# Optimization experiments

Hardware: AMD Instinct MI355X
Metric: run time of the kernel (lower is better)

Reference implementation:

```python
import jax, jax.numpy as jnp
import numpy as np

E, H, PV, RD, NS, SP, T = 4, 64, 300, 64, 8, 6, 2
N = 5000
IN_GRU = 2 * E * H  # 512


def layer_norm(x, g, b, eps=1e-5):
    m = jnp.mean(x, axis=-1, keepdims=True)
    v = jnp.var(x, axis=-1, keepdims=True)
    return (x - m) * jax.lax.rsqrt(v + eps) * g + b


def setup_inputs() -> dict:
    key = jax.random.key(0)
    ks = jax.random.split(key, 32)
    s = 0.05
    inp = {
        'adjacency_matrix': (jax.random.uniform(ks[0], (E, N, N), jnp.float32) < 0.01).astype(jnp.float32),
        'node_states': jax.random.normal(ks[1], (N, NS), jnp.float32),
        'node_ids': jnp.arange(N, dtype=jnp.int32),
        'node_vectors': jax.random.normal(ks[2], (N, PV), jnp.float32),
        'node_size_and_pos': jax.random.normal(ks[3], (N, SP), jnp.float32),
        # reduce_dimentionality: Linear(300,64)+Tanh
        'W_red': jax.random.normal(ks[4], (PV, RD), jnp.float32) * s,
        'b_red': jnp.zeros((RD,), jnp.float32),
        # node_init2hidden: Linear(64+8+6,64)+Tanh
        'W_init': jax.random.normal(ks[5], (RD + NS + SP, H), jnp.float32) * s,
        'b_init': jnp.zeros((H,), jnp.float32),
        # per-edge-type message FCs (stacked over edge types)
        'W_out': jax.random.normal(ks[6], (E, H, H), jnp.float32) * s,
        'b_out': jnp.zeros((E, H), jnp.float32),
        'W_in_e': jax.random.normal(ks[7], (E, H, H), jnp.float32) * s,
        'b_in_e': jnp.zeros((E, H), jnp.float32),
        # LayerNormGRUCell(2*E*H, H)
        'W_ih_rz': jax.random.normal(ks[8], (IN_GRU, 2 * H), jnp.float32) * s,
        'b_ih_rz': jnp.zeros((2 * H,), jnp.float32),
        'W_hh_rz': jax.random.normal(ks[9], (H, 2 * H), jnp.float32) * s,
        'b_hh_rz': jnp.zeros((2 * H,), jnp.float32),
        'W_ih_c': jax.random.normal(ks[10], (IN_GRU, H), jnp.float32) * s,
        'b_ih_c': jnp.zeros((H,), jnp.float32),
        'W_hh_c': jax.random.normal(ks[11], (H, H), jnp.float32) * s,
        'b_hh_c': jnp.zeros((H,), jnp.float32),
        'g_i2h': jnp.ones((2 * H,), jnp.float32), 'be_i2h': jnp.zeros((2 * H,), jnp.float32),
        'g_h2h': jnp.ones((2 * H,), jnp.float32), 'be_h2h': jnp.zeros((2 * H,), jnp.float32),
        'g_ci': jnp.ones((H,), jnp.float32), 'be_ci': jnp.zeros((H,), jnp.float32),
        'g_ch': jnp.ones((H,), jnp.float32), 'be_ch': jnp.zeros((H,), jnp.float32),
    }
    return inp


def _messages(A, h, W, b):
    # per-edge-type FC + tanh: [E,N,H]
    hs = jnp.tanh(jnp.einsum('nh,ehk->enk', h, W) + b[:, None, :])
    # adjacency matmul per edge type: [E,N,N] @ [E,N,H] -> [E,N,H]
    m = jnp.einsum('enm,emh->enh', A, hs)
    # torch.stack(list,1).view(N,-1) == [N, E*H]
    return jnp.transpose(m, (1, 0, 2)).reshape(h.shape[0], E * H)


def reference(adjacency_matrix, node_states, node_ids, node_vectors, node_size_and_pos,
              W_red, b_red, W_init, b_init, W_out, b_out, W_in_e, b_in_e,
              W_ih_rz, b_ih_rz, W_hh_rz, b_hh_rz, W_ih_c, b_ih_c, W_hh_c, b_hh_c,
              g_i2h, be_i2h, g_h2h, be_h2h, g_ci, be_ci, g_ch, be_ch):
    emb = jnp.tanh(node_vectors @ W_red + b_red)                      # [N,RD]
    node_init = jnp.concatenate([emb, node_states, node_size_and_pos], axis=1)
    h = jnp.tanh(node_init @ W_init + b_init)                          # [N,H]
    A_out = adjacency_matrix
    A_in = jnp.transpose(adjacency_matrix, (0, 2, 1))
    for _ in range(T):
        m_out = _messages(A_out, h, W_out, b_out)                      # [N,E*H]
        m_in = _messages(A_in, h, W_in_e, b_in_e)                      # [N,E*H]
        msg = jnp.concatenate([m_out, m_in], axis=1)                   # [N,2EH]
        # LayerNormGRUCell
        rz = jax.nn.sigmoid(layer_norm(msg @ W_ih_rz + b_ih_rz, g_i2h, be_i2h)
                            + layer_norm(h @ W_hh_rz + b_hh_rz, g_h2h, be_h2h))
        r, z = rz[:, :H], rz[:, H:]
        c = jnp.tanh(layer_norm(msg @ W_ih_c + b_ih_c, g_ci, be_ci)
                     + r * layer_norm(h @ W_hh_c + b_hh_c, g_ch, be_ch))
        h = z * h + (1.0 - z) * c
    return h
```

## Files before the change

kernel.cpp:

```cpp
#include <hip/hip_runtime.h>
#include <math.h>

#define N    5000
#define E    4
#define H    64
#define PV   300
#define RD   64
#define NS_  8
#define SP_  6
#define NI   (RD + NS_ + SP_)
#define GH   (2 * H)
#define MSGW (2 * E * H)
#define CAP  128
#define NPB  8
#define MSG_BPS 256

#define PK_S0 ((MSGW / 4) * GH)
#define PK_S1 ((MSGW / 4) * H)
#define PK_S2 ((H / 4) * GH)
#define PK_S3 ((H / 4) * H)
#define PK_TOT (PK_S0 + PK_S1 + PK_S2 + PK_S3)

#define PRE_PACK_B 108
#define PRE_ZERO_B 40
#define PRE_INIT_B 313
#define PRE_GRID (PRE_PACK_B + PRE_ZERO_B + PRE_INIT_B)

__device__ __forceinline__ float wsum(float v) {
    v += __shfl_xor(v, 32, 64);
    v += __shfl_xor(v, 16, 64);
    v += __shfl_xor(v, 8, 64);
    v += __shfl_xor(v, 4, 64);
    v += __shfl_xor(v, 2, 64);
    v += __shfl_xor(v, 1, 64);
    return v;
}

__global__ __launch_bounds__(256) void k_pre(
    const float* __restrict__ Wih_rz, const float* __restrict__ Wih_c,
    const float* __restrict__ Whh_rz, const float* __restrict__ Whh_c,
    float4* __restrict__ Prz, float4* __restrict__ Pc,
    float4* __restrict__ Phrz, float4* __restrict__ Phc,
    int4* __restrict__ cnts,
    const float* __restrict__ NV, const float* __restrict__ NSt,
    const float* __restrict__ SPos, const float* __restrict__ Wred,
    const float* __restrict__ bred, const float* __restrict__ Winit,
    const float* __restrict__ binit, float* __restrict__ h)
{
    __shared__ float nv[16 * PV];
    __shared__ float ni[16 * NI];
    const int b = blockIdx.x;
    const int tid = threadIdx.x;

    if (b < PRE_PACK_B) {
        const int i = b * 256 + tid;
        if (i < PK_S0) {
            const int kq = i / GH, col = i - kq * GH;
            Prz[i] = make_float4(Wih_rz[(4 * kq + 0) * GH + col],
                                 Wih_rz[(4 * kq + 1) * GH + col],
                                 Wih_rz[(4 * kq + 2) * GH + col],
                                 Wih_rz[(4 * kq + 3) * GH + col]);
        } else if (i < PK_S0 + PK_S1) {
            const int t = i - PK_S0;
            const int kq = t / H, col = t - kq * H;
            Pc[t] = make_float4(Wih_c[(4 * kq + 0) * H + col],
                                Wih_c[(4 * kq + 1) * H + col],
                                Wih_c[(4 * kq + 2) * H + col],
                                Wih_c[(4 * kq + 3) * H + col]);
        } else if (i < PK_S0 + PK_S1 + PK_S2) {
            const int t = i - PK_S0 - PK_S1;
            const int kq = t / GH, col = t - kq * GH;
            Phrz[t] = make_float4(Whh_rz[(4 * kq + 0) * GH + col],
                                  Whh_rz[(4 * kq + 1) * GH + col],
                                  Whh_rz[(4 * kq + 2) * GH + col],
                                  Whh_rz[(4 * kq + 3) * GH + col]);
        } else {
            const int t = i - PK_S0 - PK_S1 - PK_S2;
            const int kq = t / H, col = t - kq * H;
            Phc[t] = make_float4(Whh_c[(4 * kq + 0) * H + col],
                                 Whh_c[(4 * kq + 1) * H + col],
                                 Whh_c[(4 * kq + 2) * H + col],
                                 Whh_c[(4 * kq + 3) * H + col]);
        }
    } else if (b < PRE_PACK_B + PRE_ZERO_B) {
        const int i = (b - PRE_PACK_B) * 256 + tid;
        if (i < (2 * E * N) / 4) cnts[i] = make_int4(0, 0, 0, 0);
    } else {
        const int n0 = (b - PRE_PACK_B - PRE_ZERO_B) * 16;
        const int j = tid & 63;
        const int w = tid >> 6;
        const int nb = w * 4;

        for (int idx = tid; idx < 16 * PV; idx += 256) {
            const int n = n0 + idx / PV;
            nv[idx] = (n < N) ? NV[(size_t)n0 * PV + idx] : 0.f;
        }
        __syncthreads();

        float acc[4];
        {
            const float br = bred[j];
            #pragma unroll
            for (int nn = 0; nn < 4; ++nn) acc[nn] = br;
        }
        for (int k = 0; k < PV; ++k) {
            const float wg = Wred[k * RD + j];
            #pragma unroll
            for (int nn = 0; nn < 4; ++nn) acc[nn] += nv[(nb + nn) * PV + k] * wg;
        }
        #pragma unroll
        for (int nn = 0; nn < 4; ++nn) ni[(nb + nn) * NI + j] = tanhf(acc[nn]);
        if (j < NS_) {
            #pragma unroll
            for (int nn = 0; nn < 4; ++nn) {
                const int n = n0 + nb + nn;
                ni[(nb + nn) * NI + RD + j] = (n < N) ? NSt[(size_t)n * NS_ + j] : 0.f;
            }
        }
        if (j < SP_) {
            #pragma unroll
            for (int nn = 0; nn < 4; ++nn) {
                const int n = n0 + nb + nn;
                ni[(nb + nn) * NI + RD + NS_ + j] = (n < N) ? SPos[(size_t)n * SP_ + j] : 0.f;
            }
        }
        __syncthreads();

        float a2[4];
        {
            const float bi = binit[j];
            #pragma unroll
            for (int nn = 0; nn < 4; ++nn) a2[nn] = bi;
        }
        for (int k = 0; k < NI; ++k) {
            const float wg = Winit[k * H + j];
            #pragma unroll
            for (int nn = 0; nn < 4; ++nn) a2[nn] += ni[(nb + nn) * NI + k] * wg;
        }
        #pragma unroll
        for (int nn = 0; nn < 4; ++nn) {
            const int n = n0 + nb + nn;
            if (n < N) h[(size_t)n * H + j] = tanhf(a2[nn]);
        }
    }
}

__global__ __launch_bounds__(256) void k_build(
    const float* __restrict__ A, int* __restrict__ cnt_out, int* __restrict__ cnt_in,
    unsigned short* __restrict__ idx_out, unsigned short* __restrict__ idx_in)
{
    const int r = blockIdx.x;
    const int e = r / N;
    const int n = r - e * N;
    __shared__ int s_cnt;
    __shared__ int s_cols[CAP];
    if (threadIdx.x == 0) s_cnt = 0;
    __syncthreads();

    const float4* row = (const float4*)(A + (size_t)r * N);
    const int lane = threadIdx.x & 63;
    #pragma unroll
    for (int it = 0; it < 3; ++it) {
        const int c0 = threadIdx.x + it * 512;
        const int c1 = c0 + 256;
        float4 v0 = make_float4(0.f, 0.f, 0.f, 0.f);
        float4 v1 = make_float4(0.f, 0.f, 0.f, 0.f);
        if (c0 < N / 4) v0 = row[c0];
        if (c1 < N / 4) v1 = row[c1];
        #pragma unroll
        for (int half = 0; half < 2; ++half) {
            const float4 v = half ? v1 : v0;
            const int c = half ? c1 : c0;
            #pragma unroll
            for (int comp = 0; comp < 4; ++comp) {
                const float val = (comp == 0) ? v.x : (comp == 1) ? v.y : (comp == 2) ? v.z : v.w;
                const bool p = (val != 0.f);
                const unsigned long long m = __ballot(p);
                if (m) {
                    int base = 0;
                    if (lane == 0) base = atomicAdd(&s_cnt, (int)__popcll(m));
                    base = __shfl(base, 0, 64);
                    if (p) {
                        const int pos = base + (int)__popcll(m & ((1ull << lane) - 1ull));
                        if (pos < CAP) s_cols[pos] = 4 * c + comp;
                    }
                }
            }
        }
    }
    __syncthreads();
    const int cnt = min(s_cnt, CAP);
    if (threadIdx.x == 0) cnt_out[r] = cnt;
    for (int i = threadIdx.x; i < cnt; i += 256)
        idx_out[(size_t)r * CAP + i] = (unsigned short)s_cols[i];
    for (int i = threadIdx.x; i < cnt; i += 256) {
        const int m = s_cols[i];
        const int p = atomicAdd(&cnt_in[e * N + m], 1);
        if (p < CAP) idx_in[(size_t)(e * N + m) * CAP + p] = (unsigned short)n;
    }
}

__global__ __launch_bounds__(256) void k_hs(
    const float* __restrict__ h, const float* __restrict__ Wout,
    const float* __restrict__ bout, const float* __restrict__ Win,
    const float* __restrict__ bin, float* __restrict__ hs_out,
    float* __restrict__ hs_in)
{
    __shared__ float hsd[8 * H];
    const int n0 = blockIdx.x * 8;
    const int tid = threadIdx.x;
    const int e = tid >> 6, j = tid & 63;

    for (int idx = tid; idx < 8 * H; idx += 256) hsd[idx] = h[(size_t)n0 * H + idx];
    __syncthreads();

    float aO[8], aI[8];
    {
        const float bO = bout[e * H + j], bI = bin[e * H + j];
        #pragma unroll
        for (int nn = 0; nn < 8; ++nn) { aO[nn] = bO; aI[nn] = bI; }
    }
    for (int k = 0; k < H; ++k) {
        const float wo = Wout[(e * H + k) * H + j];
        const float wi = Win[(e * H + k) * H + j];
        #pragma unroll
        for (int nn = 0; nn < 8; ++nn) {
            const float hv = hsd[nn * H + k];
            aO[nn] += hv * wo;
            aI[nn] += hv * wi;
        }
    }
    #pragma unroll
    for (int nn = 0; nn < 8; ++nn) {
        hs_out[((size_t)e * N + n0 + nn) * H + j] = tanhf(aO[nn]);
        hs_in[((size_t)e * N + n0 + nn) * H + j]  = tanhf(aI[nn]);
    }
}

__global__ __launch_bounds__(256) void k_msg(
    const float* __restrict__ hs_out, const float* __restrict__ hs_in,
    const int* __restrict__ cnt_out, const int* __restrict__ cnt_in,
    const unsigned short* __restrict__ idx_out, const unsigned short* __restrict__ idx_in,
    float* __restrict__ msg)
{
    const int slice = blockIdx.x & 7;
    const int sb = blockIdx.x >> 3;
    const int dir = slice >> 2;
    const int e = slice & 3;
    const int tid = threadIdx.x;
    const int wv = tid >> 6;
    const int lane = tid & 63;
    const int g = lane >> 4;
    const int l = lane & 15;

    const float4* hs4 = (const float4*)((dir ? hs_in : hs_out) + (size_t)e * N * H);
    const int* cnt = (dir ? cnt_in : cnt_out) + e * N;
    const unsigned short* idx = (dir ? idx_in : idx_out) + (size_t)e * N * CAP;
    float4* mdst = (float4*)msg;

    for (int n = sb * 4 + wv; n < N; n += MSG_BPS * 4) {
        const int c = min(cnt[n], CAP);
        const unsigned short* lst = idx + (size_t)n * CAP;

        float ax = 0.f, ay = 0.f, az = 0.f, aw = 0.f;
        int i = g;
        for (; i + 12 < c; i += 16) {
            const int m0 = lst[i];
            const int m1 = lst[i + 4];
            const int m2 = lst[i + 8];
            const int m3 = lst[i + 12];
            const float4 v0 = hs4[(size_t)m0 * (H / 4) + l];
            const float4 v1 = hs4[(size_t)m1 * (H / 4) + l];
            const float4 v2 = hs4[(size_t)m2 * (H / 4) + l];
            const float4 v3 = hs4[(size_t)m3 * (H / 4) + l];
            ax += (v0.x + v1.x) + (v2.x + v3.x);
            ay += (v0.y + v1.y) + (v2.y + v3.y);
            az += (v0.z + v1.z) + (v2.z + v3.z);
            aw += (v0.w + v1.w) + (v2.w + v3.w);
        }
        for (; i < c; i += 4) {
            const float4 v = hs4[(size_t)lst[i] * (H / 4) + l];
            ax += v.x; ay += v.y; az += v.z; aw += v.w;
        }

        ax += __shfl_xor(ax, 16, 64); ay += __shfl_xor(ay, 16, 64);
        az += __shfl_xor(az, 16, 64); aw += __shfl_xor(aw, 16, 64);
        ax += __shfl_xor(ax, 32, 64); ay += __shfl_xor(ay, 32, 64);
        az += __shfl_xor(az, 32, 64); aw += __shfl_xor(aw, 32, 64);

        if (g == 0) {
            mdst[(size_t)n * (MSGW / 4) + dir * (E * H / 4) + e * (H / 4) + l] =
                make_float4(ax, ay, az, aw);
        }
    }
}

__global__ __launch_bounds__(256) void k_gru(
    const float* __restrict__ msg, const float* __restrict__ h,
    const float4* __restrict__ Prz, const float4* __restrict__ Pc,
    const float4* __restrict__ Phrz, const float4* __restrict__ Phc,
    const float* __restrict__ bih_rz, const float* __restrict__ bhh_rz,
    const float* __restrict__ bih_c, const float* __restrict__ bhh_c,
    const float* __restrict__ g_i2h, const float* __restrict__ be_i2h,
    const float* __restrict__ g_h2h, const float* __restrict__ be_h2h,
    const float* __restrict__ g_ci, const float* __restrict__ be_ci,
    const float* __restrict__ g_ch, const float* __restrict__ be_ch,
    float* __restrict__ h_out,
    const float* __restrict__ Wout, const float* __restrict__ bout,
    const float* __restrict__ Win, const float* __restrict__ bin,
    float* __restrict__ hs_out, float* __restrict__ hs_in,
    const int write_hs)
{
    __shared__ float pb[2][64][12];
    __shared__ float hn[NPB][H];
    const int n0 = blockIdx.x * NPB;
    const int tid = threadIdx.x;
    const int j = tid & 63;
    const int wv = __builtin_amdgcn_readfirstlane(tid >> 6);
    const int kh = wv & 1;
    const int q  = wv >> 1;
    const int nb = q * 4;

    const float4* ms4 = (const float4*)msg;
    const float4* hg4 = (const float4*)h;

    float a0[4], a1[4], c0[4];
    {
        const float v0 = kh ? 0.f : bih_rz[j];
        const float v1 = kh ? 0.f : bih_rz[H + j];
        const float vc = kh ? 0.f : bih_c[j];
        #pragma unroll
        for (int i = 0; i < 4; ++i) { a0[i] = v0; a1[i] = v1; c0[i] = vc; }
    }
    {
        const int kq0 = kh * (MSGW / 8);
        #pragma unroll 2
        for (int t = 0; t < MSGW / 8; ++t) {
            const int kq = kq0 + t;
            const float4 w0 = Prz[kq * GH + j];
            const float4 w1 = Prz[kq * GH + 64 + j];
            const float4 wc = Pc[kq * H + j];
            #pragma unroll
            for (int i = 0; i < 4; ++i) {
                const float4 m = ms4[(size_t)(n0 + nb + i) * (MSGW / 4) + kq];
                a0[i] += m.x * w0.x; a0[i] += m.y * w0.y;
                a0[i] += m.z * w0.z; a0[i] += m.w * w0.w;
                a1[i] += m.x * w1.x; a1[i] += m.y * w1.y;
                a1[i] += m.z * w1.z; a1[i] += m.w * w1.w;
                c0[i] += m.x * wc.x; c0[i] += m.y * wc.y;
                c0[i] += m.z * wc.z; c0[i] += m.w * wc.w;
            }
        }
    }

    float b0[4], b1[4], ch[4];
    {
        const float v0 = kh ? 0.f : bhh_rz[j];
        const float v1 = kh ? 0.f : bhh_rz[H + j];
        const float vc = kh ? 0.f : bhh_c[j];
        #pragma unroll
        for (int i = 0; i < 4; ++i) { b0[i] = v0; b1[i] = v1; ch[i] = vc; }
    }
    {
        const int kq0 = kh * (H / 8);
        #pragma unroll 2
        for (int t = 0; t < H / 8; ++t) {
            const int kq = kq0 + t;
            const float4 w0 = Phrz[kq * GH + j];
            const float4 w1 = Phrz[kq * GH + 64 + j];
            const float4 wc = Phc[kq * H + j];
            #pragma unroll
            for (int i = 0; i < 4; ++i) {
                const float4 m = hg4[(size_t)(n0 + nb + i) * (H / 4) + kq];
                b0[i] += m.x * w0.x; b0[i] += m.y * w0.y;
                b0[i] += m.z * w0.z; b0[i] += m.w * w0.w;
                b1[i] += m.x * w1.x; b1[i] += m.y * w1.y;
                b1[i] += m.z * w1.z; b1[i] += m.w * w1.w;
                ch[i] += m.x * wc.x; ch[i] += m.y * wc.y;
                ch[i] += m.z * wc.z; ch[i] += m.w * wc.w;
            }
        }
    }

    if (kh == 1) {
        #pragma unroll
        for (int i = 0; i < 4; ++i) {
            pb[q][j][i]     = a0[i];
            pb[q][j][4 + i] = a1[i];
            pb[q][j][8 + i] = c0[i];
        }
    }
    __syncthreads();
    if (kh == 0) {
        #pragma unroll
        for (int i = 0; i < 4; ++i) {
            a0[i] += pb[q][j][i];
            a1[i] += pb[q][j][4 + i];
            c0[i] += pb[q][j][8 + i];
        }
    }
    __syncthreads();
    if (kh == 1) {
        #pragma unroll
        for (int i = 0; i < 4; ++i) {
            pb[q][j][i]     = b0[i];
            pb[q][j][4 + i] = b1[i];
            pb[q][j][8 + i] = ch[i];
        }
    }
    __syncthreads();

    if (kh == 0) {
        #pragma unroll
        for (int i = 0; i < 4; ++i) {
            b0[i] += pb[q][j][i];
            b1[i] += pb[q][j][4 + i];
            ch[i] += pb[q][j][8 + i];
        }

        const float gi0 = g_i2h[j], gi1 = g_i2h[H + j], bi0 = be_i2h[j], bi1 = be_i2h[H + j];
        const float gh0 = g_h2h[j], gh1 = g_h2h[H + j], bh0 = be_h2h[j], bh1 = be_h2h[H + j];
        const float gci = g_ci[j], bci = be_ci[j], gchv = g_ch[j], bchv = be_ch[j];

        #pragma unroll
        for (int i = 0; i < 4; ++i) {
            float s  = wsum(a0[i] + a1[i]);
            float q_ = wsum(a0[i] * a0[i] + a1[i] * a1[i]);
            float mn = s * (1.f / GH);
            float vr = q_ * (1.f / GH) - mn * mn;
            float rs = rsqrtf(vr + 1e-5f);
            float x0 = (a0[i] - mn) * rs * gi0 + bi0;
            float x1 = (a1[i] - mn) * rs * gi1 + bi1;
            float s2  = wsum(b0[i] + b1[i]);
            float q2  = wsum(b0[i] * b0[i] + b1[i] * b1[i]);
            float mn2 = s2 * (1.f / GH);
            float vr2 = q2 * (1.f / GH) - mn2 * mn2;
            float rs2 = rsqrtf(vr2 + 1e-5f);
            float y0 = (b0[i] - mn2) * rs2 * gh0 + bh0;
            float y1 = (b1[i] - mn2) * rs2 * gh1 + bh1;
            const float r_ = 1.f / (1.f + expf(-(x0 + y0)));
            const float z_ = 1.f / (1.f + expf(-(x1 + y1)));

            float s3  = wsum(c0[i]);
            float q3  = wsum(c0[i] * c0[i]);
            float mn3 = s3 * (1.f / H);
            float vr3 = q3 * (1.f / H) - mn3 * mn3;
            float rs3 = rsqrtf(vr3 + 1e-5f);
            float xc = (c0[i] - mn3) * rs3 * gci + bci;
            float s4  = wsum(ch[i]);
            float q4  = wsum(ch[i] * ch[i]);
            float mn4 = s4 * (1.f / H);
            float vr4 = q4 * (1.f / H) - mn4 * mn4;
            float rs4 = rsqrtf(vr4 + 1e-5f);
            float hc = (ch[i] - mn4) * rs4 * gchv + bchv;
            float c  = tanhf(xc + r_ * hc);
            const int n = n0 + nb + i;
            const float hp = h[(size_t)n * H + j];
            const float hv = z_ * hp + (1.f - z_) * c;
            h_out[(size_t)n * H + j] = hv;
            hn[nb + i][j] = hv;
        }
    }
    __syncthreads();

    if (write_hs) {
        const int e = wv;
        float aO[8], aI[8];
        {
            const float bO = bout[e * H + j], bI = bin[e * H + j];
            #pragma unroll
            for (int nn = 0; nn < 8; ++nn) { aO[nn] = bO; aI[nn] = bI; }
        }
        for (int k = 0; k < H; ++k) {
            const float wo = Wout[(e * H + k) * H + j];
            const float wi = Win[(e * H + k) * H + j];
            #pragma unroll
            for (int nn = 0; nn < 8; ++nn) {
                const float hv = hn[nn][k];
                aO[nn] += hv * wo;
                aI[nn] += hv * wi;
            }
        }
        #pragma unroll
        for (int nn = 0; nn < 8; ++nn) {
            hs_out[((size_t)e * N + n0 + nn) * H + j] = tanhf(aO[nn]);
            hs_in[((size_t)e * N + n0 + nn) * H + j]  = tanhf(aI[nn]);
        }
    }
}

extern "C" void kernel_launch(void* const* d_in, const int* in_sizes, int n_in,
                              void* d_out, int out_size, void* d_ws, size_t ws_size,
                              hipStream_t stream)
{
    const float* A      = (const float*)d_in[0];
    const float* nstate = (const float*)d_in[1];
    const float* nvec   = (const float*)d_in[3];
    const float* nsp    = (const float*)d_in[4];
    const float* Wred   = (const float*)d_in[5];
    const float* bred   = (const float*)d_in[6];
    const float* Winit  = (const float*)d_in[7];
    const float* binit  = (const float*)d_in[8];
    const float* Wout   = (const float*)d_in[9];
    const float* bout   = (const float*)d_in[10];
    const float* Wine   = (const float*)d_in[11];
    const float* bine   = (const float*)d_in[12];
    const float* Wih_rz = (const float*)d_in[13];
    const float* bih_rz = (const float*)d_in[14];
    const float* Whh_rz = (const float*)d_in[15];
    const float* bhh_rz = (const float*)d_in[16];
    const float* Wih_c  = (const float*)d_in[17];
    const float* bih_c  = (const float*)d_in[18];
    const float* Whh_c  = (const float*)d_in[19];
    const float* bhh_c  = (const float*)d_in[20];
    const float* g_i2h  = (const float*)d_in[21];
    const float* be_i2h = (const float*)d_in[22];
    const float* g_h2h  = (const float*)d_in[23];
    const float* be_h2h = (const float*)d_in[24];
    const float* g_ci   = (const float*)d_in[25];
    const float* be_ci  = (const float*)d_in[26];
    const float* g_ch   = (const float*)d_in[27];
    const float* be_ch  = (const float*)d_in[28];

    char* ws = (char*)d_ws;
    size_t off = 0;
    auto alloc = [&](size_t bytes) {
        void* p = ws + off;
        off += (bytes + 255) & ~(size_t)255;
        return p;
    };
    float* h0  = (float*)alloc((size_t)N * H * 4);
    float* h1  = (float*)alloc((size_t)N * H * 4);
    float* hsO = (float*)alloc((size_t)E * N * H * 4);
    float* hsI = (float*)alloc((size_t)E * N * H * 4);
    float* msg = (float*)alloc((size_t)N * MSGW * 4);
    int* cnts  = (int*)alloc((size_t)2 * E * N * 4);
    int* cnt_out = cnts;
    int* cnt_in  = cnts + E * N;
    unsigned short* idxO = (unsigned short*)alloc((size_t)E * N * CAP * 2);
    unsigned short* idxI = (unsigned short*)alloc((size_t)E * N * CAP * 2);
    float4* Prz  = (float4*)alloc((size_t)PK_S0 * 16);
    float4* Pc   = (float4*)alloc((size_t)PK_S1 * 16);
    float4* Phrz = (float4*)alloc((size_t)PK_S2 * 16);
    float4* Phc  = (float4*)alloc((size_t)PK_S3 * 16);

    k_pre<<<PRE_GRID, 256, 0, stream>>>(Wih_rz, Wih_c, Whh_rz, Whh_c,
                                        Prz, Pc, Phrz, Phc, (int4*)cnts,
                                        nvec, nstate, nsp, Wred, bred, Winit, binit, h0);
    k_build<<<E * N, 256, 0, stream>>>(A, cnt_out, cnt_in, idxO, idxI);
    k_hs<<<N / 8, 256, 0, stream>>>(h0, Wout, bout, Wine, bine, hsO, hsI);

    k_msg<<<8 * MSG_BPS, 256, 0, stream>>>(hsO, hsI, cnt_out, cnt_in, idxO, idxI, msg);
    k_gru<<<N / NPB, 256, 0, stream>>>(
        msg, h0, Prz, Pc, Phrz, Phc,
        bih_rz, bhh_rz, bih_c, bhh_c,
        g_i2h, be_i2h, g_h2h, be_h2h,
        g_ci, be_ci, g_ch, be_ch, h1,
        Wout, bout, Wine, bine, hsO, hsI, 1);

    k_msg<<<8 * MSG_BPS, 256, 0, stream>>>(hsO, hsI, cnt_out, cnt_in, idxO, idxI, msg);
    k_gru<<<N / NPB, 256, 0, stream>>>(
        msg, h1, Prz, Pc, Phrz, Phc,
        bih_rz, bhh_rz, bih_c, bhh_c,
        g_i2h, be_i2h, g_h2h, be_h2h,
        g_ci, be_ci, g_ch, be_ch, (float*)d_out,
        Wout, bout, Wine, bine, hsO, hsI, 0);
}
```

Measured before the change: 282.3 us.

## Fuse per-edge hidden transform into init kernel and use wave-per-row adjacency scan

```diff
diff --git a/kernel.cpp b/kernel.cpp
--- a/kernel.cpp
+++ b/kernel.cpp
@@ -45,10 +45,14 @@
     const float* __restrict__ NV, const float* __restrict__ NSt,
     const float* __restrict__ SPos, const float* __restrict__ Wred,
     const float* __restrict__ bred, const float* __restrict__ Winit,
-    const float* __restrict__ binit, float* __restrict__ h)
+    const float* __restrict__ binit, float* __restrict__ h,
+    const float* __restrict__ Wout, const float* __restrict__ bout,
+    const float* __restrict__ Win, const float* __restrict__ bin,
+    float* __restrict__ hs_out, float* __restrict__ hs_in)
 {
     __shared__ float nv[16 * PV];
     __shared__ float ni[16 * NI];
+    __shared__ float hn[16][H];
     const int b = blockIdx.x;
     const int tid = threadIdx.x;
 
@@ -140,7 +144,36 @@
         #pragma unroll
         for (int nn = 0; nn < 4; ++nn) {
             const int n = n0 + nb + nn;
-            if (n < N) h[(size_t)n * H + j] = tanhf(a2[nn]);
+            const float hv = tanhf(a2[nn]);
+            hn[nb + nn][j] = hv;
+            if (n < N) h[(size_t)n * H + j] = hv;
+        }
+        __syncthreads();
+
+        const int e = w;
+        float aO[16], aI[16];
+        {
+            const float bO = bout[e * H + j], bI = bin[e * H + j];
+            #pragma unroll
+            for (int nn = 0; nn < 16; ++nn) { aO[nn] = bO; aI[nn] = bI; }
+        }
+        for (int k = 0; k < H; ++k) {
+            const float wo = Wout[(e * H + k) * H + j];
+            const float wi = Win[(e * H + k) * H + j];
+            #pragma unroll
+            for (int nn = 0; nn < 16; ++nn) {
+                const float hv = hn[nn][k];
+                aO[nn] += hv * wo;
+                aI[nn] += hv * wi;
+            }
+        }
+        #pragma unroll
+        for (int nn = 0; nn < 16; ++nn) {
+            const int n = n0 + nn;
+            if (n < N) {
+                hs_out[((size_t)e * N + n) * H + j] = tanhf(aO[nn]);
+                hs_in[((size_t)e * N + n) * H + j]  = tanhf(aI[nn]);
+            }
         }
     }
 }
@@ -149,92 +182,44 @@
     const float* __restrict__ A, int* __restrict__ cnt_out, int* __restrict__ cnt_in,
     unsigned short* __restrict__ idx_out, unsigned short* __restrict__ idx_in)
 {
-    const int r = blockIdx.x;
+    __shared__ unsigned short s_cols[4][CAP];
+    __shared__ int s_cnt[4];
+    const int w = threadIdx.x >> 6;
+    const int lane = threadIdx.x & 63;
+    const int r = blockIdx.x * 4 + w;
     const int e = r / N;
     const int n = r - e * N;
-    __shared__ int s_cnt;
-    __shared__ int s_cols[CAP];
-    if (threadIdx.x == 0) s_cnt = 0;
+
+    const float4* row = (const float4*)(A + (size_t)r * N);
+    int base = 0;
+    for (int it = 0; it < 20; ++it) {
+        const int c = it * 64 + lane;
+        float4 v = make_float4(0.f, 0.f, 0.f, 0.f);
+        if (c < N / 4) v = row[c];
+        #pragma unroll
+        for (int comp = 0; comp < 4; ++comp) {
+            const float val = (comp == 0) ? v.x : (comp == 1) ? v.y : (comp == 2) ? v.z : v.w;
+            const bool p = (val != 0.f);
+            const unsigned long long m = __ballot(p);
+            if (p) {
+                const int pos = base + (int)__popcll(m & ((1ull << lane) - 1ull));
+                if (pos < CAP) s_cols[w][pos] = (unsigned short)(4 * c + comp);
+            }
+            base += (int)__popcll(m);
+        }
+    }
+    const int cnt = min(base, CAP);
+    if (lane == 0) s_cnt[w] = cnt;
     __syncthreads();
 
-    const float4* row = (const float4*)(A + (size_t)r * N);
-    const int lane = threadIdx.x & 63;
-    #pragma unroll
-    for (int it = 0; it < 3; ++it) {
-        const int c0 = threadIdx.x + it * 512;
-        const int c1 = c0 + 256;
-        float4 v0 = make_float4(0.f, 0.f, 0.f, 0.f);
-        float4 v1 = make_float4(0.f, 0.f, 0.f, 0.f);
-        if (c0 < N / 4) v0 = row[c0];
-        if (c1 < N / 4) v1 = row[c1];
-        #pragma unroll
-        for (int half = 0; half < 2; ++half) {
-            const float4 v = half ? v1 : v0;
-            const int c = half ? c1 : c0;
-            #pragma unroll
-            for (int comp = 0; comp < 4; ++comp) {
-                const float val = (comp == 0) ? v.x : (comp == 1) ? v.y : (comp == 2) ? v.z : v.w;
-                const bool p = (val != 0.f);
-                const unsigned long long m = __ballot(p);
-                if (m) {
-                    int base = 0;
-                    if (lane == 0) base = atomicAdd(&s_cnt, (int)__popcll(m));
-                    base = __shfl(base, 0, 64);
-                    if (p) {
-                        const int pos = base + (int)__popcll(m & ((1ull << lane) - 1ull));
-                        if (pos < CAP) s_cols[pos] = 4 * c + comp;
-                    }
-                }
-            }
-        }
-    }
-    __syncthreads();
-    const int cnt = min(s_cnt, CAP);
-    if (threadIdx.x == 0) cnt_out[r] = cnt;
-    for (int i = threadIdx.x; i < cnt; i += 256)
-        idx_out[(size_t)r * CAP + i] = (unsigned short)s_cols[i];
-    for (int i = threadIdx.x; i < cnt; i += 256) {
-        const int m = s_cols[i];
+    const int cw = s_cnt[w];
+    for (int i = lane; i < cw; i += 64) {
+        const unsigned short m = s_cols[w][i];
+        idx_out[(size_t)r * CAP + i] = m;
         const int p = atomicAdd(&cnt_in[e * N + m], 1);
         if (p < CAP) idx_in[(size_t)(e * N + m) * CAP + p] = (unsigned short)n;
     }
-}
-
-__global__ __launch_bounds__(256) void k_hs(
-    const float* __restrict__ h, const float* __restrict__ Wout,
-    const float* __restrict__ bout, const float* __restrict__ Win,
-    const float* __restrict__ bin, float* __restrict__ hs_out,
-    float* __restrict__ hs_in)
-{
-    __shared__ float hsd[8 * H];
-    const int n0 = blockIdx.x * 8;
-    const int tid = threadIdx.x;
-    const int e = tid >> 6, j = tid & 63;
-
-    for (int idx = tid; idx < 8 * H; idx += 256) hsd[idx] = h[(size_t)n0 * H + idx];
-    __syncthreads();
-
-    float aO[8], aI[8];
-    {
-        const float bO = bout[e * H + j], bI = bin[e * H + j];
-        #pragma unroll
-        for (int nn = 0; nn < 8; ++nn) { aO[nn] = bO; aI[nn] = bI; }
-    }
-    for (int k = 0; k < H; ++k) {
-        const float wo = Wout[(e * H + k) * H + j];
-        const float wi = Win[(e * H + k) * H + j];
-        #pragma unroll
-        for (int nn = 0; nn < 8; ++nn) {
-            const float hv = hsd[nn * H + k];
-            aO[nn] += hv * wo;
-            aI[nn] += hv * wi;
-        }
-    }
-    #pragma unroll
-    for (int nn = 0; nn < 8; ++nn) {
-        hs_out[((size_t)e * N + n0 + nn) * H + j] = tanhf(aO[nn]);
-        hs_in[((size_t)e * N + n0 + nn) * H + j]  = tanhf(aI[nn]);
-    }
+    if (lane == 0) cnt_out[r] = cw;
 }
 
 __global__ __launch_bounds__(256) void k_msg(
@@ -546,9 +531,9 @@
 
     k_pre<<<PRE_GRID, 256, 0, stream>>>(Wih_rz, Wih_c, Whh_rz, Whh_c,
                                         Prz, Pc, Phrz, Phc, (int4*)cnts,
-                                        nvec, nstate, nsp, Wred, bred, Winit, binit, h0);
-    k_build<<<E * N, 256, 0, stream>>>(A, cnt_out, cnt_in, idxO, idxI);
-    k_hs<<<N / 8, 256, 0, stream>>>(h0, Wout, bout, Wine, bine, hsO, hsI);
+                                        nvec, nstate, nsp, Wred, bred, Winit, binit, h0,
+                                        Wout, bout, Wine, bine, hsO, hsI);
+    k_build<<<E * N / 4, 256, 0, stream>>>(A, cnt_out, cnt_in, idxO, idxI);
 
     k_msg<<<8 * MSG_BPS, 256, 0, stream>>>(hsO, hsI, cnt_out, cnt_in, idxO, idxI, msg);
     k_gru<<<N / NPB, 256, 0, stream>>>(
```

Measured after the change: 299.4 us. +6.0%, slower.
